# Kernel optimization log

Hardware: AMD Instinct MI355X
Metric: run time of the kernel (lower is better)

Reference implementation:

```python
import jax, jax.numpy as jnp
import numpy as np

B, T, C, H = 4, 2048, 1024, 16
D = C // H  # head_dim = 64

def setup_inputs() -> dict:
    key = jax.random.key(0)
    k1, k2, k3 = jax.random.split(key, 3)
    x = jax.random.normal(k1, (B, T, C), dtype=jnp.float32)
    W_attn = jax.random.normal(k2, (C, 3 * C), dtype=jnp.float32) * (C ** -0.5)
    b_attn = jnp.zeros((3 * C,), dtype=jnp.float32)
    W_proj = jax.random.normal(k3, (C, C), dtype=jnp.float32) * (C ** -0.5)
    b_proj = jnp.zeros((C,), dtype=jnp.float32)
    return {"x": x, "W_attn": W_attn, "b_attn": b_attn, "W_proj": W_proj, "b_proj": b_proj}

def reference(x, W_attn, b_attn, W_proj, b_proj):
    Bc, Tc, Cc = x.shape
    qkv = x @ W_attn + b_attn                       # [B,T,3C]
    q, k, v = jnp.split(qkv, 3, axis=-1)
    q = q.reshape(Bc, Tc, H, D).transpose(0, 2, 1, 3)  # [B,H,T,D]
    k = k.reshape(Bc, Tc, H, D).transpose(0, 2, 1, 3)
    v = v.reshape(Bc, Tc, H, D).transpose(0, 2, 1, 3)
    scores = jnp.einsum('bhqd,bhkd->bhqk', q, k) / jnp.sqrt(jnp.float32(D))
    causal = jnp.tril(jnp.ones((Tc, Tc), dtype=bool))
    scores = jnp.where(causal[None, None, :, :], scores, jnp.float32(-jnp.inf))
    wei = jax.nn.softmax(scores, axis=-1)           # dropout=0 -> identity
    out = jnp.einsum('bhqk,bhkd->bhqd', wei, v)     # [B,H,T,D]
    out = out.transpose(0, 2, 1, 3).reshape(Bc, Tc, Cc)
    return out @ W_proj + b_proj
```

## Files before the change

kernel.cpp:

```cpp
#include <hip/hip_runtime.h>
#include <cstdint>
#include <cstddef>

#define Bsz   4
#define Tsz   2048
#define Csz   1024
#define Hn    16
#define Dh    64
#define Mrows 8192
#define KD    1024

#define NEG_BIG (-1.0e30f)

typedef unsigned short u16;
typedef __bf16  bf16x8 __attribute__((ext_vector_type(8)));
typedef float   f32x4  __attribute__((ext_vector_type(4)));

__device__ __forceinline__ float bf2f(u16 u) {
  union { unsigned int i; float f; } v; v.i = ((unsigned int)u) << 16; return v.f;
}
__device__ __forceinline__ u16 f2bf(float f) {
  union { float f; unsigned int i; } v; v.f = f;
  unsigned int u = v.i;
  return (u16)((u + 0x7fffu + ((u >> 16) & 1u)) >> 16);
}

__global__ __launch_bounds__(256)
void cvt_f32_bf16(const float* __restrict__ in, u16* __restrict__ out, int n4) {
  const int i = blockIdx.x * 256 + threadIdx.x;
  if (i >= n4) return;
  const float4 v = ((const float4*)in)[i];
  ushort4 o;
  o.x = f2bf(v.x); o.y = f2bf(v.y); o.z = f2bf(v.z); o.w = f2bf(v.w);
  ((ushort4*)out)[i] = o;
}

__global__ __launch_bounds__(256)
void transpose_f32_bf16(const float* __restrict__ in, u16* __restrict__ out,
                        int rows, int cols) {
  __shared__ u16 tile[64][65];
  const int tc = blockIdx.x * 64, tr = blockIdx.y * 64;
  const int x = threadIdx.x & 63, y0 = threadIdx.x >> 6;
#pragma unroll
  for (int yy = 0; yy < 64; yy += 4) {
    int r = yy + y0;
    tile[r][x] = f2bf(in[(size_t)(tr + r) * cols + tc + x]);
  }
  __syncthreads();
#pragma unroll
  for (int yy = 0; yy < 64; yy += 4) {
    int r = yy + y0;
    out[(size_t)(tc + r) * rows + tr + x] = tile[x][r];
  }
}

template<int MODE>
__global__ __launch_bounds__(256)
void gemm_bt(const u16* __restrict__ A, const u16* __restrict__ BT,
             const float* __restrict__ bias, u16* __restrict__ o0,
             u16* __restrict__ o1, u16* __restrict__ o2,
             float* __restrict__ fout, int N) {
  __shared__ u16 lsA[128 * 32];
  __shared__ u16 lsB[128 * 32];
  const int tid  = threadIdx.x;
  const int lane = tid & 63;
  const int wid  = tid >> 6;
  const int wm   = wid & 1, wn = wid >> 1;
  const int quad = lane >> 4, l15 = lane & 15;
  const int m0 = blockIdx.y * 128, n0 = blockIdx.x * 128;

  f32x4 acc[4][4];
#pragma unroll
  for (int i = 0; i < 4; ++i)
#pragma unroll
    for (int j = 0; j < 4; ++j) acc[i][j] = (f32x4){0.f, 0.f, 0.f, 0.f};

#if __has_builtin(__builtin_amdgcn_global_load_lds)
  const int srow = lane >> 2, schunk = lane & 3;
  const u16* gA = A  + (size_t)(m0 + wid * 32 + srow) * KD + schunk * 8;
  const u16* gB = BT + (size_t)(n0 + wid * 32 + srow) * KD + schunk * 8;
  u16* lA0 = &lsA[(wid * 32) * 32];
  u16* lB0 = &lsB[(wid * 32) * 32];
#endif

  for (int kk = 0; kk < KD; kk += 32) {
#if __has_builtin(__builtin_amdgcn_global_load_lds)
#pragma unroll
    for (int i = 0; i < 2; ++i) {
      __builtin_amdgcn_global_load_lds(
          (const __attribute__((address_space(1))) void*)(gA + (size_t)i * 16 * KD + kk),
          (__attribute__((address_space(3))) void*)(lA0 + i * 16 * 32), 16, 0, 0);
      __builtin_amdgcn_global_load_lds(
          (const __attribute__((address_space(1))) void*)(gB + (size_t)i * 16 * KD + kk),
          (__attribute__((address_space(3))) void*)(lB0 + i * 16 * 32), 16, 0, 0);
    }
#else
#pragma unroll
    for (int cc = 0; cc < 2; ++cc) {
      int c = tid + cc * 256;
      int row = c >> 2, ch = c & 3;
      *(uint4*)&lsA[row * 32 + ch * 8] =
          *(const uint4*)&A[(size_t)(m0 + row) * KD + kk + ch * 8];
      *(uint4*)&lsB[row * 32 + ch * 8] =
          *(const uint4*)&BT[(size_t)(n0 + row) * KD + kk + ch * 8];
    }
#endif
    __syncthreads();
    bf16x8 af[4], bfv[4];
#pragma unroll
    for (int i = 0; i < 4; ++i)
      af[i] = *(const bf16x8*)&lsA[(wm * 64 + i * 16 + l15) * 32 + quad * 8];
#pragma unroll
    for (int j = 0; j < 4; ++j)
      bfv[j] = *(const bf16x8*)&lsB[(wn * 64 + j * 16 + l15) * 32 + quad * 8];
#pragma unroll
    for (int i = 0; i < 4; ++i)
#pragma unroll
      for (int j = 0; j < 4; ++j)
        acc[i][j] = __builtin_amdgcn_mfma_f32_16x16x32_bf16(af[i], bfv[j],
                                                            acc[i][j], 0, 0, 0);
    __syncthreads();
  }

#pragma unroll
  for (int i = 0; i < 4; ++i) {
#pragma unroll
    for (int j = 0; j < 4; ++j) {
      const int colb = n0 + wn * 64 + j * 16 + l15;
      const float bv = bias[colb];
#pragma unroll
      for (int r = 0; r < 4; ++r) {
        const int row = m0 + wm * 64 + i * 16 + quad * 4 + r;
        const float val = acc[i][j][r] + bv;
        if (MODE == 0) {
          const int b = row >> 11, t = row & (Tsz - 1);
          const int region = colb >> 10;
          const int nc = colb & (Csz - 1);
          const int h = nc >> 6, d = nc & 63;
          u16* dst = (region == 0) ? o0 : (region == 1) ? o1 : o2;
          dst[(size_t)(((b << 4) + h) * Tsz + t) * Dh + d] = f2bf(val);
        } else {
          fout[(size_t)row * N + colb] = val;
        }
      }
    }
  }
}

__global__ __launch_bounds__(256)
void attn_fused(const u16* __restrict__ qb, const u16* __restrict__ kbuf,
                const u16* __restrict__ vb, u16* __restrict__ outp) {
  __shared__ u16 Kl[64 * 72];
  __shared__ u16 Vt[64 * 76];
  const int tid = threadIdx.x, lane = tid & 63, w = tid >> 6;
  const int quad = lane >> 4, l15 = lane & 15;
  const int bh = blockIdx.x;
  const int jq = 31 - blockIdx.y;
  const int b = bh >> 4, h = bh & 15;
  const size_t base = (size_t)bh * Tsz * Dh;
  const u16* Q  = qb   + base;
  const u16* Kg = kbuf + base;
  const u16* Vg = vb   + base;

  const int qrow = jq * 64 + w * 16 + l15;
  const bf16x8 bq0 = *(const bf16x8*)&Q[(size_t)qrow * Dh + quad * 8];
  const bf16x8 bq1 = *(const bf16x8*)&Q[(size_t)qrow * Dh + 32 + quad * 8];

  f32x4 O[4];
#pragma unroll
  for (int nb = 0; nb < 4; ++nb) O[nb] = (f32x4){0.f, 0.f, 0.f, 0.f};
  float m_i = NEG_BIG, l_i = 0.f;

  for (int j = 0; j <= jq; ++j) {
    const int kb = j * 64;
#pragma unroll
    for (int cc = 0; cc < 2; ++cc) {
      const int c = tid + cc * 256;
      const int key = c >> 3, off = c & 7;
      *(uint4*)&Kl[key * 72 + off * 8] =
          *(const uint4*)&Kg[(size_t)(kb + key) * Dh + off * 8];
      uint4 vv = *(const uint4*)&Vg[(size_t)(kb + key) * Dh + off * 8];
      const u16* pv = (const u16*)&vv;
#pragma unroll
      for (int e = 0; e < 8; ++e) Vt[(off * 8 + e) * 76 + key] = pv[e];
    }
    __syncthreads();

    const bool diag = (j == jq);
    const int cmax = diag ? ((w * 16 + 15) >> 5) + 1 : 2;
    for (int c = 0; c < cmax; ++c) {
      const int k0 = c * 32;
      f32x4 S0 = (f32x4){0.f, 0.f, 0.f, 0.f};
      f32x4 S1 = (f32x4){0.f, 0.f, 0.f, 0.f};
      bf16x8 ak;
      ak = *(const bf16x8*)&Kl[(k0 + l15) * 72 + quad * 8];
      S0 = __builtin_amdgcn_mfma_f32_16x16x32_bf16(ak, bq0, S0, 0, 0, 0);
      ak = *(const bf16x8*)&Kl[(k0 + l15) * 72 + 32 + quad * 8];
      S0 = __builtin_amdgcn_mfma_f32_16x16x32_bf16(ak, bq1, S0, 0, 0, 0);
      ak = *(const bf16x8*)&Kl[(k0 + 16 + l15) * 72 + quad * 8];
      S1 = __builtin_amdgcn_mfma_f32_16x16x32_bf16(ak, bq0, S1, 0, 0, 0);
      ak = *(const bf16x8*)&Kl[(k0 + 16 + l15) * 72 + 32 + quad * 8];
      S1 = __builtin_amdgcn_mfma_f32_16x16x32_bf16(ak, bq1, S1, 0, 0, 0);

      const int key0 = kb + k0 + quad * 4;
      float s0[4], s1[4];
      if (diag) {
#pragma unroll
        for (int r = 0; r < 4; ++r) {
          s0[r] = (key0 + r      <= qrow) ? S0[r] * 0.125f : NEG_BIG;
          s1[r] = (key0 + 16 + r <= qrow) ? S1[r] * 0.125f : NEG_BIG;
        }
      } else {
#pragma unroll
        for (int r = 0; r < 4; ++r) {
          s0[r] = S0[r] * 0.125f;
          s1[r] = S1[r] * 0.125f;
        }
      }
      float mx = s0[0];
#pragma unroll
      for (int r = 1; r < 4; ++r) mx = fmaxf(mx, s0[r]);
#pragma unroll
      for (int r = 0; r < 4; ++r) mx = fmaxf(mx, s1[r]);
      mx = fmaxf(mx, __shfl_xor(mx, 16, 64));
      mx = fmaxf(mx, __shfl_xor(mx, 32, 64));
      const float mn = fmaxf(m_i, mx);
      const float alpha = __expf(m_i - mn);
      float p0[4], p1[4], rs = 0.f;
#pragma unroll
      for (int r = 0; r < 4; ++r) {
        p0[r] = __expf(s0[r] - mn);
        p1[r] = __expf(s1[r] - mn);
        rs += p0[r] + p1[r];
      }
      rs += __shfl_xor(rs, 16, 64);
      rs += __shfl_xor(rs, 32, 64);
      l_i = l_i * alpha + rs;
      m_i = mn;

      union { u16 u[8]; bf16x8 v; } pb;
#pragma unroll
      for (int r = 0; r < 4; ++r) {
        pb.u[r]     = f2bf(p0[r]);
        pb.u[4 + r] = f2bf(p1[r]);
      }
#pragma unroll
      for (int nb = 0; nb < 4; ++nb)
#pragma unroll
        for (int r = 0; r < 4; ++r) O[nb][r] *= alpha;
#pragma unroll
      for (int nb = 0; nb < 4; ++nb) {
        union { uint2 d[2]; bf16x8 v; } av;
        av.d[0] = *(const uint2*)&Vt[(nb * 16 + l15) * 76 + k0 + quad * 4];
        av.d[1] = *(const uint2*)&Vt[(nb * 16 + l15) * 76 + k0 + 16 + quad * 4];
        O[nb] = __builtin_amdgcn_mfma_f32_16x16x32_bf16(av.v, pb.v, O[nb], 0, 0, 0);
      }
    }
    __syncthreads();
  }

  const float inv = 1.0f / l_i;
#pragma unroll
  for (int nb = 0; nb < 4; ++nb) {
    ushort4 ov;
    ov.x = f2bf(O[nb][0] * inv);
    ov.y = f2bf(O[nb][1] * inv);
    ov.z = f2bf(O[nb][2] * inv);
    ov.w = f2bf(O[nb][3] * inv);
    *(ushort4*)&outp[(size_t)(b * Tsz + qrow) * Csz + h * Dh + nb * 16 + quad * 4] = ov;
  }
}

extern "C" void kernel_launch(void* const* d_in, const int* in_sizes, int n_in,
                              void* d_out, int out_size, void* d_ws, size_t ws_size,
                              hipStream_t stream) {
  const float* x      = (const float*)d_in[0];
  const float* W_attn = (const float*)d_in[1];
  const float* b_attn = (const float*)d_in[2];
  const float* W_proj = (const float*)d_in[3];
  const float* b_proj = (const float*)d_in[4];
  float* out = (float*)d_out;

  u16* ws   = (u16*)d_ws;
  u16* xbf  = ws;
  u16* qbuf = xbf  + (size_t)Mrows * Csz;
  u16* kbuf = qbuf + (size_t)Mrows * Csz;
  u16* vbuf = kbuf + (size_t)Mrows * Csz;
  u16* aout = vbuf + (size_t)Mrows * Csz;
  u16* WTa  = aout + (size_t)Mrows * Csz;
  u16* WTp  = WTa  + (size_t)Csz * 3 * Csz;

  cvt_f32_bf16<<<(Mrows * Csz / 4 + 255) / 256, 256, 0, stream>>>(
      x, xbf, Mrows * Csz / 4);
  transpose_f32_bf16<<<dim3(3 * Csz / 64, Csz / 64), 256, 0, stream>>>(
      W_attn, WTa, Csz, 3 * Csz);
  transpose_f32_bf16<<<dim3(Csz / 64, Csz / 64), 256, 0, stream>>>(
      W_proj, WTp, Csz, Csz);
  gemm_bt<0><<<dim3(3 * Csz / 128, Mrows / 128), 256, 0, stream>>>(
      xbf, WTa, b_attn, qbuf, kbuf, vbuf, nullptr, 3 * Csz);
  attn_fused<<<dim3(Bsz * Hn, Tsz / 64), 256, 0, stream>>>(
      qbuf, kbuf, vbuf, aout);
  gemm_bt<1><<<dim3(Csz / 128, Mrows / 128), 256, 0, stream>>>(
      aout, WTp, b_proj, nullptr, nullptr, nullptr, out, Csz);
}
```

Measured before the change: 300.8 us.

## Store V pre-transposed from QKV GEMM and process 64-key blocks per softmax step

The QKV GEMM epilogue now writes V in a [bh][d][t] transposed layout, so the attention kernel loads V tiles with vector copies instead of scattering 16-bit elements into shared memory. Online softmax now runs once per 64-key block instead of once per 32-key chunk, which halves the max/sum shuffle and rescale overhead. Exponentials use exp2 with the 1/sqrt(D) scale folded in. Float-to-bf16 packing uses a hardware packed-convert builtin where one is available. The trade-offs are more live registers for the 16 score values and stores of V in the GEMM epilogue that may be less coalesced.

New measurement: 273.4 us. 1.1x faster.

```diff
diff --git a/kernel.cpp b/kernel.cpp
--- a/kernel.cpp
+++ b/kernel.cpp
@@ -11,18 +11,33 @@
 #define KD    1024
 
 #define NEG_BIG (-1.0e30f)
+#define SCL2 0.18033688011112042f
 
 typedef unsigned short u16;
 typedef __bf16  bf16x8 __attribute__((ext_vector_type(8)));
+typedef __bf16  bf16x2 __attribute__((ext_vector_type(2)));
 typedef float   f32x4  __attribute__((ext_vector_type(4)));
 
-__device__ __forceinline__ float bf2f(u16 u) {
-  union { unsigned int i; float f; } v; v.i = ((unsigned int)u) << 16; return v.f;
-}
 __device__ __forceinline__ u16 f2bf(float f) {
   union { float f; unsigned int i; } v; v.f = f;
   unsigned int u = v.i;
   return (u16)((u + 0x7fffu + ((u >> 16) & 1u)) >> 16);
+}
+__device__ __forceinline__ unsigned int pack2bf(float a, float b) {
+#if __has_builtin(__builtin_amdgcn_cvt_pk_bf16_f32)
+  union { bf16x2 h; unsigned int u; } cv;
+  cv.h = __builtin_amdgcn_cvt_pk_bf16_f32(a, b);
+  return cv.u;
+#else
+  return (unsigned int)f2bf(a) | ((unsigned int)f2bf(b) << 16);
+#endif
+}
+__device__ __forceinline__ float fast_exp2(float x) {
+#if __has_builtin(__builtin_amdgcn_exp2f)
+  return __builtin_amdgcn_exp2f(x);
+#else
+  return exp2f(x);
+#endif
 }
 
 __global__ __launch_bounds__(256)
@@ -30,9 +45,10 @@
   const int i = blockIdx.x * 256 + threadIdx.x;
   if (i >= n4) return;
   const float4 v = ((const float4*)in)[i];
-  ushort4 o;
-  o.x = f2bf(v.x); o.y = f2bf(v.y); o.z = f2bf(v.z); o.w = f2bf(v.w);
-  ((ushort4*)out)[i] = o;
+  uint2 o;
+  o.x = pack2bf(v.x, v.y);
+  o.y = pack2bf(v.z, v.w);
+  ((uint2*)out)[i] = o;
 }
 
 __global__ __launch_bounds__(256)
@@ -128,20 +144,30 @@
     for (int j = 0; j < 4; ++j) {
       const int colb = n0 + wn * 64 + j * 16 + l15;
       const float bv = bias[colb];
-#pragma unroll
-      for (int r = 0; r < 4; ++r) {
-        const int row = m0 + wm * 64 + i * 16 + quad * 4 + r;
-        const float val = acc[i][j][r] + bv;
-        if (MODE == 0) {
-          const int b = row >> 11, t = row & (Tsz - 1);
-          const int region = colb >> 10;
-          const int nc = colb & (Csz - 1);
-          const int h = nc >> 6, d = nc & 63;
-          u16* dst = (region == 0) ? o0 : (region == 1) ? o1 : o2;
-          dst[(size_t)(((b << 4) + h) * Tsz + t) * Dh + d] = f2bf(val);
+      float vals[4];
+#pragma unroll
+      for (int r = 0; r < 4; ++r) vals[r] = acc[i][j][r] + bv;
+      const int row0 = m0 + wm * 64 + i * 16 + quad * 4;
+      if (MODE == 0) {
+        const int b = row0 >> 11, t0 = row0 & (Tsz - 1);
+        const int region = colb >> 10;
+        const int nc = colb & (Csz - 1);
+        const int h = nc >> 6, d = nc & 63;
+        if (region == 2) {
+          uint2 st;
+          st.x = pack2bf(vals[0], vals[1]);
+          st.y = pack2bf(vals[2], vals[3]);
+          *(uint2*)&o2[((size_t)((b << 4) + h) * Dh + d) * Tsz + t0] = st;
         } else {
-          fout[(size_t)row * N + colb] = val;
+          u16* dst = (region == 0) ? o0 : o1;
+#pragma unroll
+          for (int r = 0; r < 4; ++r)
+            dst[(size_t)(((b << 4) + h) * Tsz + t0 + r) * Dh + d] = f2bf(vals[r]);
         }
+      } else {
+#pragma unroll
+        for (int r = 0; r < 4; ++r)
+          fout[(size_t)(row0 + r) * N + colb] = vals[r];
       }
     }
   }
@@ -149,18 +175,17 @@
 
 __global__ __launch_bounds__(256)
 void attn_fused(const u16* __restrict__ qb, const u16* __restrict__ kbuf,
-                const u16* __restrict__ vb, u16* __restrict__ outp) {
+                const u16* __restrict__ vT, u16* __restrict__ outp) {
   __shared__ u16 Kl[64 * 72];
-  __shared__ u16 Vt[64 * 76];
+  __shared__ u16 Vt[64 * 72];
   const int tid = threadIdx.x, lane = tid & 63, w = tid >> 6;
   const int quad = lane >> 4, l15 = lane & 15;
   const int bh = blockIdx.x;
   const int jq = 31 - blockIdx.y;
   const int b = bh >> 4, h = bh & 15;
-  const size_t base = (size_t)bh * Tsz * Dh;
-  const u16* Q  = qb   + base;
-  const u16* Kg = kbuf + base;
-  const u16* Vg = vb   + base;
+  const u16* Q   = qb   + (size_t)bh * Tsz * Dh;
+  const u16* Kg  = kbuf + (size_t)bh * Tsz * Dh;
+  const u16* VTg = vT   + (size_t)bh * Dh * Tsz;
 
   const int qrow = jq * 64 + w * 16 + l15;
   const bf16x8 bq0 = *(const bf16x8*)&Q[(size_t)qrow * Dh + quad * 8];
@@ -176,83 +201,101 @@
 #pragma unroll
     for (int cc = 0; cc < 2; ++cc) {
       const int c = tid + cc * 256;
-      const int key = c >> 3, off = c & 7;
-      *(uint4*)&Kl[key * 72 + off * 8] =
-          *(const uint4*)&Kg[(size_t)(kb + key) * Dh + off * 8];
-      uint4 vv = *(const uint4*)&Vg[(size_t)(kb + key) * Dh + off * 8];
-      const u16* pv = (const u16*)&vv;
-#pragma unroll
-      for (int e = 0; e < 8; ++e) Vt[(off * 8 + e) * 76 + key] = pv[e];
+      const int rr = c >> 3, off = c & 7;
+      *(uint4*)&Kl[rr * 72 + off * 8] =
+          *(const uint4*)&Kg[(size_t)(kb + rr) * Dh + off * 8];
+      *(uint4*)&Vt[rr * 72 + off * 8] =
+          *(const uint4*)&VTg[(size_t)rr * Tsz + kb + off * 8];
     }
     __syncthreads();
 
     const bool diag = (j == jq);
-    const int cmax = diag ? ((w * 16 + 15) >> 5) + 1 : 2;
-    for (int c = 0; c < cmax; ++c) {
-      const int k0 = c * 32;
-      f32x4 S0 = (f32x4){0.f, 0.f, 0.f, 0.f};
-      f32x4 S1 = (f32x4){0.f, 0.f, 0.f, 0.f};
-      bf16x8 ak;
-      ak = *(const bf16x8*)&Kl[(k0 + l15) * 72 + quad * 8];
-      S0 = __builtin_amdgcn_mfma_f32_16x16x32_bf16(ak, bq0, S0, 0, 0, 0);
-      ak = *(const bf16x8*)&Kl[(k0 + l15) * 72 + 32 + quad * 8];
-      S0 = __builtin_amdgcn_mfma_f32_16x16x32_bf16(ak, bq1, S0, 0, 0, 0);
-      ak = *(const bf16x8*)&Kl[(k0 + 16 + l15) * 72 + quad * 8];
-      S1 = __builtin_amdgcn_mfma_f32_16x16x32_bf16(ak, bq0, S1, 0, 0, 0);
-      ak = *(const bf16x8*)&Kl[(k0 + 16 + l15) * 72 + 32 + quad * 8];
-      S1 = __builtin_amdgcn_mfma_f32_16x16x32_bf16(ak, bq1, S1, 0, 0, 0);
-
-      const int key0 = kb + k0 + quad * 4;
-      float s0[4], s1[4];
-      if (diag) {
-#pragma unroll
-        for (int r = 0; r < 4; ++r) {
-          s0[r] = (key0 + r      <= qrow) ? S0[r] * 0.125f : NEG_BIG;
-          s1[r] = (key0 + 16 + r <= qrow) ? S1[r] * 0.125f : NEG_BIG;
+    const int tmax = diag ? (w + 1) : 4;
+
+    f32x4 S[4];
+#pragma unroll
+    for (int t = 0; t < 4; ++t) S[t] = (f32x4){0.f, 0.f, 0.f, 0.f};
+#pragma unroll
+    for (int t = 0; t < 4; ++t) {
+      if (t < tmax) {
+        bf16x8 ak = *(const bf16x8*)&Kl[(t * 16 + l15) * 72 + quad * 8];
+        S[t] = __builtin_amdgcn_mfma_f32_16x16x32_bf16(ak, bq0, S[t], 0, 0, 0);
+        ak = *(const bf16x8*)&Kl[(t * 16 + l15) * 72 + 32 + quad * 8];
+        S[t] = __builtin_amdgcn_mfma_f32_16x16x32_bf16(ak, bq1, S[t], 0, 0, 0);
+      }
+    }
+
+    float s[4][4];
+#pragma unroll
+    for (int t = 0; t < 4; ++t)
+#pragma unroll
+      for (int r = 0; r < 4; ++r) s[t][r] = NEG_BIG;
+    if (diag) {
+#pragma unroll
+      for (int t = 0; t < 4; ++t) {
+        if (t < tmax) {
+          const int key0 = kb + t * 16 + quad * 4;
+#pragma unroll
+          for (int r = 0; r < 4; ++r)
+            s[t][r] = (key0 + r <= qrow) ? S[t][r] : NEG_BIG;
         }
-      } else {
-#pragma unroll
-        for (int r = 0; r < 4; ++r) {
-          s0[r] = S0[r] * 0.125f;
-          s1[r] = S1[r] * 0.125f;
-        }
-      }
-      float mx = s0[0];
-#pragma unroll
-      for (int r = 1; r < 4; ++r) mx = fmaxf(mx, s0[r]);
-#pragma unroll
-      for (int r = 0; r < 4; ++r) mx = fmaxf(mx, s1[r]);
-      mx = fmaxf(mx, __shfl_xor(mx, 16, 64));
-      mx = fmaxf(mx, __shfl_xor(mx, 32, 64));
-      const float mn = fmaxf(m_i, mx);
-      const float alpha = __expf(m_i - mn);
-      float p0[4], p1[4], rs = 0.f;
+      }
+    } else {
+#pragma unroll
+      for (int t = 0; t < 4; ++t)
+#pragma unroll
+        for (int r = 0; r < 4; ++r) s[t][r] = S[t][r];
+    }
+
+    float mx = s[0][0];
+#pragma unroll
+    for (int t = 0; t < 4; ++t)
+#pragma unroll
+      for (int r = 0; r < 4; ++r) mx = fmaxf(mx, s[t][r]);
+    mx = fmaxf(mx, __shfl_xor(mx, 16, 64));
+    mx = fmaxf(mx, __shfl_xor(mx, 32, 64));
+    const float mn = fmaxf(m_i, mx);
+    const float alpha = fast_exp2((m_i - mn) * SCL2);
+    float p[4][4], rs = 0.f;
+#pragma unroll
+    for (int t = 0; t < 4; ++t)
 #pragma unroll
       for (int r = 0; r < 4; ++r) {
-        p0[r] = __expf(s0[r] - mn);
-        p1[r] = __expf(s1[r] - mn);
-        rs += p0[r] + p1[r];
-      }
-      rs += __shfl_xor(rs, 16, 64);
-      rs += __shfl_xor(rs, 32, 64);
-      l_i = l_i * alpha + rs;
-      m_i = mn;
-
-      union { u16 u[8]; bf16x8 v; } pb;
-#pragma unroll
-      for (int r = 0; r < 4; ++r) {
-        pb.u[r]     = f2bf(p0[r]);
-        pb.u[4 + r] = f2bf(p1[r]);
-      }
-#pragma unroll
-      for (int nb = 0; nb < 4; ++nb)
-#pragma unroll
-        for (int r = 0; r < 4; ++r) O[nb][r] *= alpha;
+        p[t][r] = fast_exp2((s[t][r] - mn) * SCL2);
+        rs += p[t][r];
+      }
+    rs += __shfl_xor(rs, 16, 64);
+    rs += __shfl_xor(rs, 32, 64);
+    l_i = l_i * alpha + rs;
+    m_i = mn;
+
+#pragma unroll
+    for (int nb = 0; nb < 4; ++nb)
+#pragma unroll
+      for (int r = 0; r < 4; ++r) O[nb][r] *= alpha;
+
+    union PB { unsigned int u32[4]; bf16x8 v; } pb;
+    pb.u32[0] = pack2bf(p[0][0], p[0][1]);
+    pb.u32[1] = pack2bf(p[0][2], p[0][3]);
+    pb.u32[2] = pack2bf(p[1][0], p[1][1]);
+    pb.u32[3] = pack2bf(p[1][2], p[1][3]);
+#pragma unroll
+    for (int nb = 0; nb < 4; ++nb) {
+      union { uint2 d[2]; bf16x8 v; } av;
+      av.d[0] = *(const uint2*)&Vt[(nb * 16 + l15) * 72 + quad * 4];
+      av.d[1] = *(const uint2*)&Vt[(nb * 16 + l15) * 72 + 16 + quad * 4];
+      O[nb] = __builtin_amdgcn_mfma_f32_16x16x32_bf16(av.v, pb.v, O[nb], 0, 0, 0);
+    }
+    if (tmax > 2) {
+      pb.u32[0] = pack2bf(p[2][0], p[2][1]);
+      pb.u32[1] = pack2bf(p[2][2], p[2][3]);
+      pb.u32[2] = pack2bf(p[3][0], p[3][1]);
+      pb.u32[3] = pack2bf(p[3][2], p[3][3]);
 #pragma unroll
       for (int nb = 0; nb < 4; ++nb) {
         union { uint2 d[2]; bf16x8 v; } av;
-        av.d[0] = *(const uint2*)&Vt[(nb * 16 + l15) * 76 + k0 + quad * 4];
-        av.d[1] = *(const uint2*)&Vt[(nb * 16 + l15) * 76 + k0 + 16 + quad * 4];
+        av.d[0] = *(const uint2*)&Vt[(nb * 16 + l15) * 72 + 32 + quad * 4];
+        av.d[1] = *(const uint2*)&Vt[(nb * 16 + l15) * 72 + 48 + quad * 4];
         O[nb] = __builtin_amdgcn_mfma_f32_16x16x32_bf16(av.v, pb.v, O[nb], 0, 0, 0);
       }
     }
@@ -262,12 +305,10 @@
   const float inv = 1.0f / l_i;
 #pragma unroll
   for (int nb = 0; nb < 4; ++nb) {
-    ushort4 ov;
-    ov.x = f2bf(O[nb][0] * inv);
-    ov.y = f2bf(O[nb][1] * inv);
-    ov.z = f2bf(O[nb][2] * inv);
-    ov.w = f2bf(O[nb][3] * inv);
-    *(ushort4*)&outp[(size_t)(b * Tsz + qrow) * Csz + h * Dh + nb * 16 + quad * 4] = ov;
+    uint2 st;
+    st.x = pack2bf(O[nb][0] * inv, O[nb][1] * inv);
+    st.y = pack2bf(O[nb][2] * inv, O[nb][3] * inv);
+    *(uint2*)&outp[(size_t)(b * Tsz + qrow) * Csz + h * Dh + nb * 16 + quad * 4] = st;
   }
 }
 
```
